# Optimization experiments

Measured on AMD Instinct MI355X. Metric: run time of the kernel, lower is better.

## Reference

```python
import jax, jax.numpy as jnp
import numpy as np

E = 1024      # embed_dim (== embed_dim_)
NH = 8        # num_heads
HD = E // NH  # head_dim
BS1 = 2048
BS2 = 2048
EPS = 1e-5


def _layernorm(x, g, b):
    m = jnp.mean(x, axis=-1, keepdims=True)
    v = jnp.mean(jnp.square(x - m), axis=-1, keepdims=True)
    return (x - m) * jax.lax.rsqrt(v + EPS) * g + b


def setup_inputs() -> dict:
    key = jax.random.key(0)
    ks = jax.random.split(key, 16)
    s = 1.0 / np.sqrt(E)
    s4 = 1.0 / np.sqrt(4 * E)
    inp = {
        "x1": jax.random.normal(ks[0], (BS1, E), jnp.float32),
        "x2": jax.random.normal(ks[1], (BS2, E), jnp.float32),
        "Wq": jax.random.uniform(ks[2], (E, E), jnp.float32, -s, s),
        "bq": jax.random.uniform(ks[3], (E,), jnp.float32, -s, s),
        "Wk": jax.random.uniform(ks[4], (E, E), jnp.float32, -s, s),
        "bk": jax.random.uniform(ks[5], (E,), jnp.float32, -s, s),
        "Wv": jax.random.uniform(ks[6], (E, E), jnp.float32, -s, s),
        "bv": jax.random.uniform(ks[7], (E,), jnp.float32, -s, s),
        "Wo": jax.random.uniform(ks[8], (E, E), jnp.float32, -s, s),
        "bo": jax.random.uniform(ks[9], (E,), jnp.float32, -s, s),
        "W1": jax.random.uniform(ks[10], (4 * E, E), jnp.float32, -s, s),
        "b1": jax.random.uniform(ks[11], (4 * E,), jnp.float32, -s, s),
        "W2": jax.random.uniform(ks[12], (E, 4 * E), jnp.float32, -s4, s4),
        "b2": jax.random.uniform(ks[13], (E,), jnp.float32, -s4, s4),
        "g1": jnp.ones((E,), jnp.float32),
        "be1": jnp.zeros((E,), jnp.float32),
        "g2": jnp.ones((E,), jnp.float32),
        "be2": jnp.zeros((E,), jnp.float32),
    }
    return inp


def reference(x1, x2, Wq, bq, Wk, bk, Wv, bv, Wo, bo, W1, b1, W2, b2, g1, be1, g2, be2):
    scale = HD ** -0.5
    # Projections; attention runs over the batch axis (n=bs1, m=bs2)
    q = (x1 @ Wq.T + bq).reshape(BS1, NH, HD)   # [n,h,d]
    k = (x2 @ Wk.T + bk).reshape(BS2, NH, HD)   # [m,h,d]
    v = (x2 @ Wv.T + bv).reshape(BS2, NH, HD)   # [m,h,d]
    scores = jnp.einsum('nhd,mhd->nmh', q, k) * scale  # [n,m,h]
    # NOTE: faithful to source: softmax over the HEADS axis (dim=-1)
    probs = jax.nn.softmax(scores, axis=-1)
    # dropout is identity in eval mode
    attn = jnp.einsum('nmh,mhd->nhd', probs, v).reshape(BS1, E)
    attn = attn @ Wo.T + bo
    h = _layernorm(x1 + attn, g1, be1)
    ffn = jax.nn.relu(h @ W1.T + b1) @ W2.T + b2
    return _layernorm(h + ffn, g2, be2)
```

## Files before the change

### kernel.cpp

```cpp
#include <hip/hip_runtime.h>

#define BS 2048
#define EMB 1024
#define NHEAD 8
#define HDIM 128

typedef unsigned short u16;
typedef __attribute__((ext_vector_type(8))) short bf16x8;
typedef __attribute__((ext_vector_type(4))) float f32x4;

__device__ __forceinline__ u16 f32_bf16(float f) {
  unsigned u = __float_as_uint(f);
  u += 0x7fffu + ((u >> 16) & 1u);
  return (u16)(u >> 16);
}
__device__ __forceinline__ float bf2f(u16 x) {
  return __uint_as_float((unsigned)x << 16);
}

__device__ __forceinline__ void gld_lds16(const void* g, void* l) {
  __builtin_amdgcn_global_load_lds(
      (const __attribute__((address_space(1))) void*)g,
      (__attribute__((address_space(3))) void*)l, 16, 0, 0);
}

struct CvtArgs { const float* src[8]; };
__global__ __launch_bounds__(256) void cvt_all(CvtArgs a, u16* __restrict__ dst) {
  long i = (long)blockIdx.x * 256 + threadIdx.x;
  int seg = (int)(i >> 18);
  const float* src; long b;
  if (seg < 2)       { src = a.src[0]; b = 0; }
  else if (seg < 4)  { src = a.src[1]; b = 2L << 18; }
  else if (seg == 4) { src = a.src[2]; b = 4L << 18; }
  else if (seg == 5) { src = a.src[3]; b = 5L << 18; }
  else if (seg == 6) { src = a.src[4]; b = 6L << 18; }
  else if (seg == 7) { src = a.src[5]; b = 7L << 18; }
  else if (seg < 12) { src = a.src[6]; b = 8L << 18; }
  else               { src = a.src[7]; b = 12L << 18; }
  float4 v = ((const float4*)src)[i - b];
  ushort4 o;
  o.x = f32_bf16(v.x); o.y = f32_bf16(v.y); o.z = f32_bf16(v.z); o.w = f32_bf16(v.w);
  ((ushort4*)dst)[i] = o;
}

__device__ __forceinline__ void gemm_core(
    const u16* __restrict__ A, const u16* __restrict__ B, void* __restrict__ Cp,
    const float* __restrict__ bias, int K, int lda, int ldb, int ldc,
    long cbase, int mode, int relu, int m0, int n0) {
  __shared__ __align__(16) u16 As[128 * 32];
  __shared__ __align__(16) u16 Bs[128 * 32];
  const int t = threadIdx.x;
  const int lane = t & 63, l15 = lane & 15, quad = lane >> 4;
  const int wv = t >> 6, wr = wv & 1, wc = wv >> 1;
  const int wbase = t & ~63;

  f32x4 acc[4][4];
#pragma unroll
  for (int r = 0; r < 4; ++r)
#pragma unroll
    for (int c = 0; c < 4; ++c) acc[r][c] = (f32x4){0.f, 0.f, 0.f, 0.f};

  for (int k0 = 0; k0 < K; k0 += 32) {
#pragma unroll
    for (int i = 0; i < 2; ++i) {
      int s = i * 256 + t;
      gld_lds16(A + (long)(m0 + (s >> 2)) * lda + k0 + (s & 3) * 8,
                As + (i * 256 + wbase) * 8);
    }
#pragma unroll
    for (int i = 0; i < 2; ++i) {
      int s = i * 256 + t;
      gld_lds16(B + (long)(n0 + (s >> 2)) * ldb + k0 + (s & 3) * 8,
                Bs + (i * 256 + wbase) * 8);
    }
    __syncthreads();
    bf16x8 fa[4], fb[4];
#pragma unroll
    for (int r = 0; r < 4; ++r)
      fa[r] = *(const bf16x8*)&As[(wr * 64 + r * 16 + l15) * 32 + quad * 8];
#pragma unroll
    for (int c = 0; c < 4; ++c)
      fb[c] = *(const bf16x8*)&Bs[(wc * 64 + c * 16 + l15) * 32 + quad * 8];
#pragma unroll
    for (int r = 0; r < 4; ++r)
#pragma unroll
      for (int c = 0; c < 4; ++c)
        acc[r][c] = __builtin_amdgcn_mfma_f32_16x16x32_bf16(fa[r], fb[c], acc[r][c], 0, 0, 0);
    __syncthreads();
  }

#pragma unroll
  for (int r = 0; r < 4; ++r)
#pragma unroll
    for (int c = 0; c < 4; ++c) {
      const int m = m0 + wr * 64 + r * 16 + quad * 4;
      const int n = n0 + wc * 64 + c * 16 + l15;
      const float bv = bias ? bias[n] : 0.f;
      f32x4 v = acc[r][c];
      if (mode == 2) {
        ushort4 o;
        o.x = f32_bf16(v[0] + bv);
        o.y = f32_bf16(v[1] + bv);
        o.z = f32_bf16(v[2] + bv);
        o.w = f32_bf16(v[3] + bv);
        *(ushort4*)((u16*)Cp + cbase + (long)n * ldc + m) = o;
      } else {
#pragma unroll
        for (int i = 0; i < 4; ++i) {
          float x = v[i] + bv;
          if (relu) x = fmaxf(x, 0.f);
          if (mode == 0)
            ((float*)Cp)[cbase + (long)(m + i) * ldc + n] = x;
          else
            ((u16*)Cp)[cbase + (long)(m + i) * ldc + n] = f32_bf16(x);
        }
      }
    }
}

__global__ __launch_bounds__(256) void gemm_bt_k(
    const u16* __restrict__ A, const u16* __restrict__ B, void* __restrict__ C,
    const float* __restrict__ bias, int K, int lda, int ldb, int ldc,
    long aOffZ, long bOffZ, long cOffZ, int mode, int relu) {
  gemm_core(A + (long)blockIdx.z * aOffZ, B + (long)blockIdx.z * bOffZ, C, bias,
            K, lda, ldb, ldc, (long)blockIdx.z * cOffZ, mode, relu,
            blockIdx.y * 128, blockIdx.x * 128);
}

__global__ __launch_bounds__(256) void qkv_kernel(
    const u16* __restrict__ x1b, const u16* __restrict__ x2b,
    const u16* __restrict__ Wqb, const u16* __restrict__ Wkb, const u16* __restrict__ Wvb,
    const float* __restrict__ bq, const float* __restrict__ bk, const float* __restrict__ bv,
    u16* __restrict__ Qb, u16* __restrict__ Kb, u16* __restrict__ Vt) {
  const int z = blockIdx.z;
  const u16* A = (z == 0) ? x1b : x2b;
  const u16* B = (z == 0) ? Wqb : (z == 1) ? Wkb : Wvb;
  void* C = (z == 0) ? (void*)Qb : (z == 1) ? (void*)Kb : (void*)Vt;
  const float* bias = (z == 0) ? bq : (z == 1) ? bk : bv;
  const int mode = (z == 2) ? 2 : 1;
  const int ldc = (z == 2) ? 2048 : 1024;
  gemm_core(A, B, C, bias, 1024, 1024, 1024, ldc, 0, mode, 0,
            blockIdx.y * 128, blockIdx.x * 128);
}

__global__ __launch_bounds__(256) void pv_kernel(
    const u16* __restrict__ P, const u16* __restrict__ Vt,
    u16* p0, u16* p1, u16* p2, u16* p3) {
  const int h = blockIdx.z >> 2, ks = blockIdx.z & 3;
  u16* parts = (ks == 0) ? p0 : (ks == 1) ? p1 : (ks == 2) ? p2 : p3;
  const u16* A = P + (long)h * BS * BS + ks * 512;
  const u16* B = Vt + (long)h * HDIM * 2048 + ks * 512;
  gemm_core(A, B, parts, nullptr, 512, 2048, 2048, 1024, (long)h * HDIM, 1, 0,
            blockIdx.y * 128, 0);
}

__global__ __launch_bounds__(256) void reduce4p_bf16(
    const u16* __restrict__ p0, const u16* __restrict__ p1,
    const u16* __restrict__ p2, const u16* __restrict__ p3, u16* __restrict__ out) {
  long i = (long)blockIdx.x * 256 + threadIdx.x;
  ushort4 a = ((const ushort4*)p0)[i];
  ushort4 b = ((const ushort4*)p1)[i];
  ushort4 c = ((const ushort4*)p2)[i];
  ushort4 d = ((const ushort4*)p3)[i];
  ushort4 o;
  o.x = f32_bf16(bf2f(a.x) + bf2f(b.x) + bf2f(c.x) + bf2f(d.x));
  o.y = f32_bf16(bf2f(a.y) + bf2f(b.y) + bf2f(c.y) + bf2f(d.y));
  o.z = f32_bf16(bf2f(a.z) + bf2f(b.z) + bf2f(c.z) + bf2f(d.z));
  o.w = f32_bf16(bf2f(a.w) + bf2f(b.w) + bf2f(c.w) + bf2f(d.w));
  ((ushort4*)out)[i] = o;
}

__global__ __launch_bounds__(256) void scores_softmax(
    const u16* __restrict__ Q, const u16* __restrict__ Km, u16* __restrict__ P) {
  __shared__ __align__(16) u16 Qs[2][4096];
  __shared__ __align__(16) u16 Ks[2][16384];
  const int t = threadIdx.x;
  const int lane = t & 63, l15 = lane & 15, quad = lane >> 4;
  const int wv = t >> 6, wbase = t & ~63;
  const int n0 = blockIdx.y * 32, m0 = blockIdx.x * 128;

  auto stage = [&](int h, int b) {
#pragma unroll
    for (int i = 0; i < 2; ++i) {
      int s = i * 256 + t;
      gld_lds16(Q + (long)(n0 + ((s >> 2) & 31)) * EMB + h * HDIM + (s >> 7) * 32 + (s & 3) * 8,
                &Qs[b][(i * 256 + wbase) * 8]);
    }
#pragma unroll
    for (int i = 0; i < 8; ++i) {
      int s = i * 256 + t;
      gld_lds16(Km + (long)(m0 + ((s >> 2) & 127)) * EMB + h * HDIM + (s >> 9) * 32 + (s & 3) * 8,
                &Ks[b][(i * 256 + wbase) * 8]);
    }
  };

  f32x4 acc[8][2][2];
#pragma unroll
  for (int h = 0; h < 8; ++h)
#pragma unroll
    for (int r = 0; r < 2; ++r)
#pragma unroll
      for (int c = 0; c < 2; ++c) acc[h][r][c] = (f32x4){0.f, 0.f, 0.f, 0.f};

  stage(0, 0);
#pragma unroll
  for (int h = 0; h < 8; ++h) {
    __syncthreads();
    if (h < 7) stage(h + 1, (h + 1) & 1);
    const u16* qb = Qs[h & 1];
    const u16* kb = Ks[h & 1];
#pragma unroll
    for (int kk = 0; kk < 4; ++kk) {
      bf16x8 fa[2], fb[2];
#pragma unroll
      for (int r = 0; r < 2; ++r)
        fa[r] = *(const bf16x8*)&qb[kk * 1024 + (r * 16 + l15) * 32 + quad * 8];
#pragma unroll
      for (int c = 0; c < 2; ++c)
        fb[c] = *(const bf16x8*)&kb[kk * 4096 + (wv * 32 + c * 16 + l15) * 32 + quad * 8];
#pragma unroll
      for (int r = 0; r < 2; ++r)
#pragma unroll
        for (int c = 0; c < 2; ++c)
          acc[h][r][c] = __builtin_amdgcn_mfma_f32_16x16x32_bf16(fa[r], fb[c], acc[h][r][c], 0, 0, 0);
    }
  }

  const float scale = 0.08838834764831845f;
#pragma unroll
  for (int r = 0; r < 2; ++r)
#pragma unroll
    for (int c = 0; c < 2; ++c)
#pragma unroll
      for (int i = 0; i < 4; ++i) {
        float mx = acc[0][r][c][i];
#pragma unroll
        for (int h = 1; h < 8; ++h) mx = fmaxf(mx, acc[h][r][c][i]);
        float sum = 0.f;
#pragma unroll
        for (int h = 0; h < 8; ++h) {
          float e = __expf((acc[h][r][c][i] - mx) * scale);
          acc[h][r][c][i] = e;
          sum += e;
        }
        float inv = 1.f / sum;
#pragma unroll
        for (int h = 0; h < 8; ++h) acc[h][r][c][i] *= inv;
      }

#pragma unroll
  for (int h = 0; h < 8; ++h) {
    u16* ph = P + (long)h * BS * BS;
#pragma unroll
    for (int r = 0; r < 2; ++r)
#pragma unroll
      for (int c = 0; c < 2; ++c)
#pragma unroll
        for (int i = 0; i < 4; ++i)
          ph[(long)(n0 + r * 16 + quad * 4 + i) * BS + m0 + wv * 32 + c * 16 + l15] =
              f32_bf16(acc[h][r][c][i]);
  }
}

__global__ __launch_bounds__(256) void ln_residual_p4(
    const float* __restrict__ x,
    const u16* __restrict__ p0, const u16* __restrict__ p1,
    const u16* __restrict__ p2, const u16* __restrict__ p3,
    const float* __restrict__ colb, const float* __restrict__ g, const float* __restrict__ b,
    float* __restrict__ out32, u16* __restrict__ out16) {
  const int row = blockIdx.x, t = threadIdx.x;
  const long base = (long)row * EMB;
  float4 v = ((const float4*)(x + base))[t];
  ushort4 a0 = ((const ushort4*)(p0 + base))[t];
  ushort4 a1 = ((const ushort4*)(p1 + base))[t];
  ushort4 a2 = ((const ushort4*)(p2 + base))[t];
  ushort4 a3 = ((const ushort4*)(p3 + base))[t];
  float4 cb = ((const float4*)colb)[t];
  v.x += bf2f(a0.x) + bf2f(a1.x) + bf2f(a2.x) + bf2f(a3.x) + cb.x;
  v.y += bf2f(a0.y) + bf2f(a1.y) + bf2f(a2.y) + bf2f(a3.y) + cb.y;
  v.z += bf2f(a0.z) + bf2f(a1.z) + bf2f(a2.z) + bf2f(a3.z) + cb.z;
  v.w += bf2f(a0.w) + bf2f(a1.w) + bf2f(a2.w) + bf2f(a3.w) + cb.w;
  float s = v.x + v.y + v.z + v.w;
  float q = v.x * v.x + v.y * v.y + v.z * v.z + v.w * v.w;
#pragma unroll
  for (int off = 32; off > 0; off >>= 1) {
    s += __shfl_xor(s, off);
    q += __shfl_xor(q, off);
  }
  __shared__ float red[8];
  const int wv = t >> 6, lane = t & 63;
  if (lane == 0) { red[wv] = s; red[4 + wv] = q; }
  __syncthreads();
  s = red[0] + red[1] + red[2] + red[3];
  q = red[4] + red[5] + red[6] + red[7];
  const float mean = s * (1.f / EMB);
  const float var = q * (1.f / EMB) - mean * mean;
  const float rstd = rsqrtf(var + 1e-5f);
  float4 gg = ((const float4*)g)[t];
  float4 bb = ((const float4*)b)[t];
  float4 o;
  o.x = (v.x - mean) * rstd * gg.x + bb.x;
  o.y = (v.y - mean) * rstd * gg.y + bb.y;
  o.z = (v.z - mean) * rstd * gg.z + bb.z;
  o.w = (v.w - mean) * rstd * gg.w + bb.w;
  ((float4*)(out32 + base))[t] = o;
  if (out16) {
    ushort4 ho;
    ho.x = f32_bf16(o.x); ho.y = f32_bf16(o.y); ho.z = f32_bf16(o.z); ho.w = f32_bf16(o.w);
    ((ushort4*)(out16 + base))[t] = ho;
  }
}

extern "C" void kernel_launch(void* const* d_in, const int* in_sizes, int n_in,
                              void* d_out, int out_size, void* d_ws, size_t ws_size,
                              hipStream_t stream) {
  const float* x1 = (const float*)d_in[0];
  const float* x2 = (const float*)d_in[1];
  const float* Wq = (const float*)d_in[2];
  const float* bq = (const float*)d_in[3];
  const float* Wk = (const float*)d_in[4];
  const float* bk = (const float*)d_in[5];
  const float* Wv = (const float*)d_in[6];
  const float* bv = (const float*)d_in[7];
  const float* Wo = (const float*)d_in[8];
  const float* bo = (const float*)d_in[9];
  const float* W1 = (const float*)d_in[10];
  const float* b1 = (const float*)d_in[11];
  const float* W2 = (const float*)d_in[12];
  const float* b2 = (const float*)d_in[13];
  const float* g1 = (const float*)d_in[14];
  const float* be1 = (const float*)d_in[15];
  const float* g2 = (const float*)d_in[16];
  const float* be2 = (const float*)d_in[17];

  char* ws = (char*)d_ws;
  const size_t MB = 1ull << 20;
  u16* x1b = (u16*)(ws + 0 * MB);
  u16* x2b = (u16*)(ws + 4 * MB);
  u16* Wqb = (u16*)(ws + 8 * MB);
  u16* Wkb = (u16*)(ws + 10 * MB);
  u16* Wvb = (u16*)(ws + 12 * MB);
  u16* Wob = (u16*)(ws + 14 * MB);
  u16* W1b = (u16*)(ws + 16 * MB);
  u16* W2b = (u16*)(ws + 24 * MB);
  u16* Qb  = (u16*)(ws + 32 * MB);
  u16* Kb  = (u16*)(ws + 36 * MB);
  u16* Vtb = (u16*)(ws + 40 * MB);
  u16* attnb = (u16*)(ws + 44 * MB);
  u16* P   = (u16*)(ws + 48 * MB);
  u16* woP[4] = {(u16*)(ws + 48 * MB), (u16*)(ws + 52 * MB),
                 (u16*)(ws + 56 * MB), (u16*)(ws + 60 * MB)};
  float* h32  = (float*)(ws + 64 * MB);
  u16*  h16   = (u16*)(ws + 72 * MB);
  u16*  ffn1b = (u16*)(ws + 76 * MB);
  u16* f2P[4] = {(u16*)(ws + 92 * MB), (u16*)(ws + 96 * MB),
                 (u16*)(ws + 100 * MB), (u16*)(ws + 104 * MB)};

  CvtArgs ca;
  ca.src[0] = x1; ca.src[1] = x2; ca.src[2] = Wq; ca.src[3] = Wk;
  ca.src[4] = Wv; ca.src[5] = Wo; ca.src[6] = W1; ca.src[7] = W2;
  cvt_all<<<16384, 256, 0, stream>>>(ca, (u16*)ws);

  qkv_kernel<<<dim3(8, 16, 3), 256, 0, stream>>>(x1b, x2b, Wqb, Wkb, Wvb, bq, bk, bv, Qb, Kb, Vtb);

  scores_softmax<<<dim3(16, 64), 256, 0, stream>>>(Qb, Kb, P);

  pv_kernel<<<dim3(1, 16, 32), 256, 0, stream>>>(P, Vtb, x1b, x2b, Qb, Kb);

  reduce4p_bf16<<<2048, 256, 0, stream>>>(x1b, x2b, Qb, Kb, attnb);

  gemm_bt_k<<<dim3(8, 16, 4), 256, 0, stream>>>(attnb, Wob, woP[0], nullptr,
                                                256, 1024, 1024, 1024,
                                                256, 256, (long)BS * 1024, 1, 0);

  ln_residual_p4<<<2048, 256, 0, stream>>>(x1, woP[0], woP[1], woP[2], woP[3],
                                           bo, g1, be1, h32, h16);

  gemm_bt_k<<<dim3(32, 16, 1), 256, 0, stream>>>(h16, W1b, ffn1b, b1,
                                                 1024, 1024, 1024, 4096,
                                                 0, 0, 0, 1, 1);

  gemm_bt_k<<<dim3(8, 16, 4), 256, 0, stream>>>(ffn1b, W2b, f2P[0], nullptr,
                                                1024, 4096, 4096, 1024,
                                                1024, 1024, (long)BS * 1024, 1, 0);

  ln_residual_p4<<<2048, 256, 0, stream>>>(h32, f2P[0], f2P[1], f2P[2], f2P[3],
                                           b2, g2, be2, (float*)d_out, nullptr);
}
```

Baseline: 340.3 us.

## Fuse attention scores, softmax and PV into one kernel keeping P in LDS

Replaces the separate scores_softmax and pv_kernel with a single fused kernel. Each block holds a 32-row Q tile in swizzled LDS, computes the scores for all 8 heads over a 128-key chunk, applies the softmax over the head axis, writes probabilities to LDS and immediately multiplies them by V. This removes the materialisation of the large bf16 probability tensor in global memory and one kernel launch. In exchange, K and V fragments are read straight from global memory without LDS staging, and the grid is small with large LDS use per block, which may limit occupancy and latency hiding.

```diff
diff --git a/kernel.cpp b/kernel.cpp
--- a/kernel.cpp
+++ b/kernel.cpp
@@ -143,15 +143,113 @@
             blockIdx.y * 128, blockIdx.x * 128);
 }
 
-__global__ __launch_bounds__(256) void pv_kernel(
-    const u16* __restrict__ P, const u16* __restrict__ Vt,
-    u16* p0, u16* p1, u16* p2, u16* p3) {
-  const int h = blockIdx.z >> 2, ks = blockIdx.z & 3;
-  u16* parts = (ks == 0) ? p0 : (ks == 1) ? p1 : (ks == 2) ? p2 : p3;
-  const u16* A = P + (long)h * BS * BS + ks * 512;
-  const u16* B = Vt + (long)h * HDIM * 2048 + ks * 512;
-  gemm_core(A, B, parts, nullptr, 512, 2048, 2048, 1024, (long)h * HDIM, 1, 0,
-            blockIdx.y * 128, 0);
+__global__ __launch_bounds__(512, 2) void attn_fused(
+    const u16* __restrict__ Q, const u16* __restrict__ Km, const u16* __restrict__ Vt,
+    u16* __restrict__ p0, u16* __restrict__ p1, u16* __restrict__ p2, u16* __restrict__ p3) {
+  __shared__ __align__(16) u16 Qs[32 * 1024];
+  __shared__ __align__(16) u16 Ps[8 * 32 * 128];
+  const int t = threadIdx.x;
+  const int lane = t & 63, l15 = lane & 15, quad = lane >> 4;
+  const int w = t >> 6, wbase = t & ~63;
+  const int n0 = blockIdx.x * 32;
+  const int mz = blockIdx.y * 512;
+  u16* part = (blockIdx.y == 0) ? p0 : (blockIdx.y == 1) ? p1 : (blockIdx.y == 2) ? p2 : p3;
+
+#pragma unroll
+  for (int i = 0; i < 8; ++i) {
+    int s = i * 512 + t;
+    int n = s >> 7;
+    int kel = (((s & 127) << 3) ^ ((n & 7) << 3));
+    gld_lds16(Q + (long)(n0 + n) * 1024 + kel, Qs + (i * 512 + wbase) * 8);
+  }
+
+  f32x4 accp[2][8];
+#pragma unroll
+  for (int r = 0; r < 2; ++r)
+#pragma unroll
+    for (int c = 0; c < 8; ++c) accp[r][c] = (f32x4){0.f, 0.f, 0.f, 0.f};
+
+  for (int it = 0; it < 4; ++it) {
+    __syncthreads();
+    f32x4 accs[8][2];
+#pragma unroll
+    for (int h = 0; h < 8; ++h)
+#pragma unroll
+      for (int c = 0; c < 2; ++c) accs[h][c] = (f32x4){0.f, 0.f, 0.f, 0.f};
+    const u16* krow = Km + (long)(mz + it * 128 + w * 16 + l15) * 1024;
+#pragma unroll
+    for (int h = 0; h < 8; ++h)
+#pragma unroll
+      for (int kk = 0; kk < 4; ++kk) {
+        bf16x8 kf = *(const bf16x8*)&krow[h * 128 + kk * 32 + quad * 8];
+#pragma unroll
+        for (int c = 0; c < 2; ++c) {
+          int n = c * 16 + l15;
+          int kel = (h * 128 + kk * 32 + quad * 8) ^ ((n & 7) << 3);
+          bf16x8 qf = *(const bf16x8*)&Qs[n * 1024 + kel];
+          accs[h][c] = __builtin_amdgcn_mfma_f32_16x16x32_bf16(kf, qf, accs[h][c], 0, 0, 0);
+        }
+      }
+    const float scale = 0.08838834764831845f;
+#pragma unroll
+    for (int c = 0; c < 2; ++c)
+#pragma unroll
+      for (int i = 0; i < 4; ++i) {
+        float mx = accs[0][c][i];
+#pragma unroll
+        for (int h = 1; h < 8; ++h) mx = fmaxf(mx, accs[h][c][i]);
+        float sum = 0.f;
+#pragma unroll
+        for (int h = 0; h < 8; ++h) {
+          float e = __expf((accs[h][c][i] - mx) * scale);
+          accs[h][c][i] = e;
+          sum += e;
+        }
+        float inv = 1.f / sum;
+#pragma unroll
+        for (int h = 0; h < 8; ++h) accs[h][c][i] *= inv;
+      }
+#pragma unroll
+    for (int h = 0; h < 8; ++h)
+#pragma unroll
+      for (int c = 0; c < 2; ++c) {
+        int n = c * 16 + l15;
+        ushort4 o;
+        o.x = f32_bf16(accs[h][c][0]);
+        o.y = f32_bf16(accs[h][c][1]);
+        o.z = f32_bf16(accs[h][c][2]);
+        o.w = f32_bf16(accs[h][c][3]);
+        int mb = (w * 32 + quad * 8) ^ ((n & 7) << 4);
+        *(ushort4*)((char*)Ps + h * 8192 + n * 256 + mb) = o;
+      }
+    __syncthreads();
+#pragma unroll
+    for (int mq = 0; mq < 4; ++mq) {
+      bf16x8 pa[2];
+#pragma unroll
+      for (int r = 0; r < 2; ++r) {
+        int n = r * 16 + l15;
+        int mb = (mq * 64 + quad * 16) ^ ((n & 7) << 4);
+        pa[r] = *(const bf16x8*)((const char*)Ps + w * 8192 + n * 256 + mb);
+      }
+#pragma unroll
+      for (int c = 0; c < 8; ++c) {
+        bf16x8 vf = *(const bf16x8*)&Vt[(long)(w * 128 + c * 16 + l15) * 2048 +
+                                        mz + it * 128 + mq * 32 + quad * 8];
+#pragma unroll
+        for (int r = 0; r < 2; ++r)
+          accp[r][c] = __builtin_amdgcn_mfma_f32_16x16x32_bf16(pa[r], vf, accp[r][c], 0, 0, 0);
+      }
+    }
+  }
+#pragma unroll
+  for (int r = 0; r < 2; ++r)
+#pragma unroll
+    for (int c = 0; c < 8; ++c)
+#pragma unroll
+      for (int i = 0; i < 4; ++i)
+        part[(long)(n0 + r * 16 + quad * 4 + i) * 1024 + w * 128 + c * 16 + l15] =
+            f32_bf16(accp[r][c][i]);
 }
 
 __global__ __launch_bounds__(256) void reduce4p_bf16(
@@ -168,98 +266,6 @@
   o.z = f32_bf16(bf2f(a.z) + bf2f(b.z) + bf2f(c.z) + bf2f(d.z));
   o.w = f32_bf16(bf2f(a.w) + bf2f(b.w) + bf2f(c.w) + bf2f(d.w));
   ((ushort4*)out)[i] = o;
-}
-
-__global__ __launch_bounds__(256) void scores_softmax(
-    const u16* __restrict__ Q, const u16* __restrict__ Km, u16* __restrict__ P) {
-  __shared__ __align__(16) u16 Qs[2][4096];
-  __shared__ __align__(16) u16 Ks[2][16384];
-  const int t = threadIdx.x;
-  const int lane = t & 63, l15 = lane & 15, quad = lane >> 4;
-  const int wv = t >> 6, wbase = t & ~63;
-  const int n0 = blockIdx.y * 32, m0 = blockIdx.x * 128;
-
-  auto stage = [&](int h, int b) {
-#pragma unroll
-    for (int i = 0; i < 2; ++i) {
-      int s = i * 256 + t;
-      gld_lds16(Q + (long)(n0 + ((s >> 2) & 31)) * EMB + h * HDIM + (s >> 7) * 32 + (s & 3) * 8,
-                &Qs[b][(i * 256 + wbase) * 8]);
-    }
-#pragma unroll
-    for (int i = 0; i < 8; ++i) {
-      int s = i * 256 + t;
-      gld_lds16(Km + (long)(m0 + ((s >> 2) & 127)) * EMB + h * HDIM + (s >> 9) * 32 + (s & 3) * 8,
-                &Ks[b][(i * 256 + wbase) * 8]);
-    }
-  };
-
-  f32x4 acc[8][2][2];
-#pragma unroll
-  for (int h = 0; h < 8; ++h)
-#pragma unroll
-    for (int r = 0; r < 2; ++r)
-#pragma unroll
-      for (int c = 0; c < 2; ++c) acc[h][r][c] = (f32x4){0.f, 0.f, 0.f, 0.f};
-
-  stage(0, 0);
-#pragma unroll
-  for (int h = 0; h < 8; ++h) {
-    __syncthreads();
-    if (h < 7) stage(h + 1, (h + 1) & 1);
-    const u16* qb = Qs[h & 1];
-    const u16* kb = Ks[h & 1];
-#pragma unroll
-    for (int kk = 0; kk < 4; ++kk) {
-      bf16x8 fa[2], fb[2];
-#pragma unroll
-      for (int r = 0; r < 2; ++r)
-        fa[r] = *(const bf16x8*)&qb[kk * 1024 + (r * 16 + l15) * 32 + quad * 8];
-#pragma unroll
-      for (int c = 0; c < 2; ++c)
-        fb[c] = *(const bf16x8*)&kb[kk * 4096 + (wv * 32 + c * 16 + l15) * 32 + quad * 8];
-#pragma unroll
-      for (int r = 0; r < 2; ++r)
-#pragma unroll
-        for (int c = 0; c < 2; ++c)
-          acc[h][r][c] = __builtin_amdgcn_mfma_f32_16x16x32_bf16(fa[r], fb[c], acc[h][r][c], 0, 0, 0);
-    }
-  }
-
-  const float scale = 0.08838834764831845f;
-#pragma unroll
-  for (int r = 0; r < 2; ++r)
-#pragma unroll
-    for (int c = 0; c < 2; ++c)
-#pragma unroll
-      for (int i = 0; i < 4; ++i) {
-        float mx = acc[0][r][c][i];
-#pragma unroll
-        for (int h = 1; h < 8; ++h) mx = fmaxf(mx, acc[h][r][c][i]);
-        float sum = 0.f;
-#pragma unroll
-        for (int h = 0; h < 8; ++h) {
-          float e = __expf((acc[h][r][c][i] - mx) * scale);
-          acc[h][r][c][i] = e;
-          sum += e;
-        }
-        float inv = 1.f / sum;
-#pragma unroll
-        for (int h = 0; h < 8; ++h) acc[h][r][c][i] *= inv;
-      }
-
-#pragma unroll
-  for (int h = 0; h < 8; ++h) {
-    u16* ph = P + (long)h * BS * BS;
-#pragma unroll
-    for (int r = 0; r < 2; ++r)
-#pragma unroll
-      for (int c = 0; c < 2; ++c)
-#pragma unroll
-        for (int i = 0; i < 4; ++i)
-          ph[(long)(n0 + r * 16 + quad * 4 + i) * BS + m0 + wv * 32 + c * 16 + l15] =
-              f32_bf16(acc[h][r][c][i]);
-  }
 }
 
 __global__ __launch_bounds__(256) void ln_residual_p4(
@@ -347,7 +353,8 @@
   u16* Kb  = (u16*)(ws + 36 * MB);
   u16* Vtb = (u16*)(ws + 40 * MB);
   u16* attnb = (u16*)(ws + 44 * MB);
-  u16* P   = (u16*)(ws + 48 * MB);
+  u16* aP[4] = {(u16*)(ws + 48 * MB), (u16*)(ws + 52 * MB),
+                (u16*)(ws + 56 * MB), (u16*)(ws + 60 * MB)};
   u16* woP[4] = {(u16*)(ws + 48 * MB), (u16*)(ws + 52 * MB),
                  (u16*)(ws + 56 * MB), (u16*)(ws + 60 * MB)};
   float* h32  = (float*)(ws + 64 * MB);
@@ -363,11 +370,9 @@
 
   qkv_kernel<<<dim3(8, 16, 3), 256, 0, stream>>>(x1b, x2b, Wqb, Wkb, Wvb, bq, bk, bv, Qb, Kb, Vtb);
 
-  scores_softmax<<<dim3(16, 64), 256, 0, stream>>>(Qb, Kb, P);
-
-  pv_kernel<<<dim3(1, 16, 32), 256, 0, stream>>>(P, Vtb, x1b, x2b, Qb, Kb);
-
-  reduce4p_bf16<<<2048, 256, 0, stream>>>(x1b, x2b, Qb, Kb, attnb);
+  attn_fused<<<dim3(64, 4), 512, 0, stream>>>(Qb, Kb, Vtb, aP[0], aP[1], aP[2], aP[3]);
+
+  reduce4p_bf16<<<2048, 256, 0, stream>>>(aP[0], aP[1], aP[2], aP[3], attnb);
 
   gemm_bt_k<<<dim3(8, 16, 4), 256, 0, stream>>>(attnb, Wob, woP[0], nullptr,
                                                 256, 1024, 1024, 1024,
```

New measurement: 336.4 us. Within noise of the previous version (-1.2%).
